# Optimization experiments

Measured on AMD Instinct MI355X. Metric: run time of the kernel, lower is better.

The kernel has to match this reference:

```python
import jax, jax.numpy as jnp
import numpy as np

B, L, D = 512, 128, 128  # batch, sequence_length (=k), embedding_dim==hidden_dim
C_CLIP = 10.0  # pointer logit clipping constant from Attention(C=10)


def _lstm_cell(x, h, c, w_ih, w_hh, b_ih, b_hh):
    # torch.nn.LSTMCell gate order: i, f, g, o
    gates = x @ w_ih.T + b_ih + h @ w_hh.T + b_hh
    i, f, g, o = jnp.split(gates, 4, axis=-1)
    c2 = jax.nn.sigmoid(f) * c + jax.nn.sigmoid(i) * jnp.tanh(g)
    h2 = jax.nn.sigmoid(o) * jnp.tanh(c2)
    return h2, c2


def setup_inputs() -> dict:
    key = jax.random.key(0)
    ks = jax.random.split(key, 16)
    s = 0.09  # ~1/sqrt(D) init scale
    return dict(
        decoder_input=jax.random.normal(ks[0], (B, D), jnp.float32),
        embedding_x=jax.random.normal(ks[1], (L, B, D), jnp.float32),
        h0=jax.random.normal(ks[2], (B, D), jnp.float32),
        c0=jax.random.normal(ks[3], (B, D), jnp.float32),
        encoder_output=jax.random.normal(ks[4], (L, B, D), jnp.float32),
        w_ih=jax.random.normal(ks[5], (4 * D, D), jnp.float32) * s,
        w_hh=jax.random.normal(ks[6], (4 * D, D), jnp.float32) * s,
        b_ih=jnp.zeros((4 * D,), jnp.float32),
        b_hh=jnp.zeros((4 * D,), jnp.float32),
        wq_p=jax.random.normal(ks[7], (D, D), jnp.float32) * s,
        bq_p=jnp.zeros((D,), jnp.float32),
        wr_p=jax.random.normal(ks[8], (D, D), jnp.float32) * s,
        br_p=jnp.zeros((D,), jnp.float32),
        v_p=jax.random.normal(ks[9], (D,), jnp.float32) * s,
        wq_g=jax.random.normal(ks[10], (D, D), jnp.float32) * s,
        bq_g=jnp.zeros((D,), jnp.float32),
        wr_g=jax.random.normal(ks[11], (D, D), jnp.float32) * s,
        br_g=jnp.zeros((D,), jnp.float32),
        v_g=jax.random.normal(ks[12], (D,), jnp.float32) * s,
    )


def _decode(decoder_input, embedding_x, h0, c0, encoder_output,
            w_ih, w_hh, b_ih, b_hh,
            wq_p, bq_p, wr_p, br_p, v_p,
            wq_g, bq_g, wr_g, br_g, v_g):
    enc = encoder_output.transpose(1, 0, 2)  # (B, L, D)
    emb = embedding_x.transpose(1, 0, 2)     # (B, L, D)
    # w_ref is a 1x1 Conv1d == per-position Linear; hoist out of the loop
    ref_p = enc @ wr_p.T + br_p              # (B, L, D) pointer refs
    ref_g = enc @ wr_g.T + br_g              # (B, L, D) glimpse refs
    barange = jnp.arange(B)

    mask0 = jnp.zeros((B, L), bool).at[:, :2].set(True)  # indices 0,1 pre-visited

    def step(carry, _):
        h, c, dec_in, mask, prev_idx, use_prev = carry
        h, c = _lstm_cell(dec_in, h, c, w_ih, w_hh, b_ih, b_hh)
        # mask_logit: only applied once prev_idx exists (i.e. after first step)
        mask_new = jnp.where(use_prev, mask.at[barange, prev_idx].set(True), mask)
        # glimpse attention (num_glimpse=1, no logit clipping)
        g = h
        u = jnp.einsum('d,bld->bl', v_g,
                       jnp.tanh(ref_g + (g @ wq_g.T + bq_g)[:, None, :]))
        u = jnp.where(use_prev & mask_new, -jnp.inf, u)
        p = jax.nn.softmax(u, axis=-1)
        g = jnp.einsum('bl,bld->bd', p, enc)  # glimpse readout uses raw encoder output
        # pointer attention (clipped logits)
        u = jnp.einsum('d,bld->bl', v_p,
                       jnp.tanh(ref_p + (g @ wq_p.T + bq_p)[:, None, :]))
        u = C_CLIP * jnp.tanh(u)
        u = jnp.where(use_prev & mask_new, -jnp.inf, u)
        probs = jax.nn.softmax(u, axis=-1)          # (B, L)
        idx = jnp.argmax(probs, axis=-1)            # greedy decode
        dec_in = emb[barange, idx]                  # (B, D)
        return (h, c, dec_in, mask_new, idx, jnp.array(True)), (probs, idx)

    init = (h0, c0, decoder_input, mask0,
            jnp.zeros((B,), jnp.int32), jnp.array(False))
    _, (probs_seq, idx_seq) = jax.lax.scan(step, init, None, length=L - 2)
    return probs_seq, idx_seq  # (L-2, B, L), (L-2, B)


def reference(decoder_input, embedding_x, h0, c0, encoder_output,
              w_ih, w_hh, b_ih, b_hh,
              wq_p, bq_p, wr_p, br_p, v_p,
              wq_g, bq_g, wr_g, br_g, v_g):
    return _decode(decoder_input, embedding_x, h0, c0, encoder_output,
                   w_ih, w_hh, b_ih, b_hh,
                   wq_p, bq_p, wr_p, br_p, v_p,
                   wq_g, bq_g, wr_g, br_g, v_g)
```

## Files before the change

### kernel.cpp

```cpp
#include <hip/hip_runtime.h>
#include <math.h>

namespace {

constexpr int kB = 512;
constexpr int kL = 128;
constexpr int kD = 128;
constexpr int kSteps = 126;

constexpr size_t OFF_WL   = 0;
constexpr size_t OFF_BIAS = 131072;
constexpr size_t OFF_WQLG = 131584;
constexpr size_t OFF_WQTP = 147968;
constexpr size_t OFF_WRTG = 164352;
constexpr size_t OFF_WRTP = 180736;
constexpr size_t OFF_WIHT = 197120;
constexpr size_t OFF_REFG = 262656;
constexpr size_t OFF_REFP = OFF_REFG + (size_t)kL * kB * kD;
constexpr size_t OFF_ENCQ = OFF_REFP + (size_t)kL * kB * kD;
constexpr size_t kTotalNoGx = OFF_ENCQ + (size_t)kL * kB * kD;
constexpr size_t OFF_GX   = kTotalNoGx;
constexpr size_t kTotalGx = OFF_GX + (size_t)129 * kB * 512;

constexpr size_t OUT_IDX_OFF = (size_t)kSteps * kB * kL;

constexpr int SM_REFP = 0;
constexpr int SM_H    = 16384;
constexpr int SM_C    = 16512;
constexpr int SM_G    = 16640;
constexpr int SM_RED  = 17152;
constexpr int SM_QG   = 17408;
constexpr int SM_U    = 17536;
constexpr int SM_PG   = 17664;
constexpr int SM_M    = 17792;
constexpr int SM_VG   = 17920;
constexpr int SM_VP   = 18048;
constexpr int SM_IDX  = 18176;
constexpr int SM_TOTAL= 18180;

__device__ __forceinline__ float tanh_fast(float x) {
  return 1.0f - __fdividef(2.0f, __expf(2.0f * x) + 1.0f);
}
__device__ __forceinline__ float sig_fast(float x) {
  return __fdividef(1.0f, 1.0f + __expf(-x));
}

#define KEEP4(v) asm volatile("" : "+v"(v.x), "+v"(v.y), "+v"(v.z), "+v"(v.w))

}

extern "C" __global__ void prep_weights(
    const float* __restrict__ w_ih, const float* __restrict__ w_hh,
    const float* __restrict__ b_ih, const float* __restrict__ b_hh,
    const float* __restrict__ wq_p, const float* __restrict__ wq_g,
    const float* __restrict__ wr_p, const float* __restrict__ wr_g,
    float* __restrict__ ws) {
  const int tid = blockIdx.x * blockDim.x + threadIdx.x;
  const int nth = gridDim.x * blockDim.x;
  for (int i = tid; i < 256 * 512; i += nth) {
    const int k = i >> 9, g = i & 511;
    ws[OFF_WL + i] = (k < 128) ? w_ih[g * 128 + k] : w_hh[g * 128 + (k - 128)];
  }
  for (int i = tid; i < 512; i += nth) ws[OFF_BIAS + i] = b_ih[i] + b_hh[i];
  for (int i = tid; i < 16384; i += nth) {
    const int e = i & 3, rest = i >> 2;
    const int kq = rest & 1, j = (rest >> 1) & 127, kk4 = rest >> 8;
    const int k = kq * 64 + kk4 * 4 + e;
    ws[OFF_WQLG + i] = wq_g[j * 128 + k];
  }
  for (int i = tid; i < 128 * 512; i += nth) {
    const int k = i >> 9, g = i & 511;
    ws[OFF_WIHT + i] = w_ih[g * 128 + k];
  }
  for (int i = tid; i < 128 * 128; i += nth) {
    const int k = i >> 7, j = i & 127;
    ws[OFF_WQTP + i] = wq_p[j * 128 + k];
    ws[OFF_WRTG + i] = wr_g[j * 128 + k];
    ws[OFF_WRTP + i] = wr_p[j * 128 + k];
  }
}

extern "C" __global__ __launch_bounds__(256) void prep_mm(
    const float* __restrict__ enc,
    const float* __restrict__ br_g, const float* __restrict__ br_p,
    const float* __restrict__ bq_p,
    float* __restrict__ ws) {
  extern __shared__ float lds[];
  float* wT = lds;
  float* sx = lds + 16384;
  const int t = threadIdx.x;
  const int table = blockIdx.y;
  const size_t wOff = (table == 0) ? OFF_WRTG : (table == 1) ? OFF_WRTP : OFF_WQTP;
  const size_t oOff = (table == 0) ? OFF_REFG : (table == 1) ? OFF_REFP : OFF_ENCQ;
  const float* bias = (table == 0) ? br_g : (table == 1) ? br_p : bq_p;
  for (int i = t; i < 16384; i += 256) wT[i] = ws[wOff + i];
  const size_t r0 = (size_t)blockIdx.x * 64;
  for (int i = t; i < 8192; i += 256) sx[i] = enc[r0 * 128 + i];
  __syncthreads();
  const int j0 = (t & 31) * 4, rg = t >> 5;
  float4 acc[8];
  const float4 b4 = *(const float4*)(bias + j0);
  #pragma unroll
  for (int r = 0; r < 8; ++r) acc[r] = b4;
  for (int k4 = 0; k4 < 32; ++k4) {
    const float4 w0 = *(const float4*)&wT[(k4 * 4 + 0) * 128 + j0];
    const float4 w1 = *(const float4*)&wT[(k4 * 4 + 1) * 128 + j0];
    const float4 w2 = *(const float4*)&wT[(k4 * 4 + 2) * 128 + j0];
    const float4 w3 = *(const float4*)&wT[(k4 * 4 + 3) * 128 + j0];
    #pragma unroll
    for (int r = 0; r < 8; ++r) {
      const float4 xv = *(const float4*)&sx[(rg * 8 + r) * 128 + k4 * 4];
      acc[r].x += xv.x * w0.x + xv.y * w1.x + xv.z * w2.x + xv.w * w3.x;
      acc[r].y += xv.x * w0.y + xv.y * w1.y + xv.z * w2.y + xv.w * w3.y;
      acc[r].z += xv.x * w0.z + xv.y * w1.z + xv.z * w2.z + xv.w * w3.z;
      acc[r].w += xv.x * w0.w + xv.y * w1.w + xv.z * w2.w + xv.w * w3.w;
    }
  }
  #pragma unroll
  for (int r = 0; r < 8; ++r) {
    *(float4*)&ws[oOff + (r0 + rg * 8 + r) * 128 + j0] = acc[r];
  }
}

extern "C" __global__ __launch_bounds__(256) void prep_gx(
    const float* __restrict__ emb, const float* __restrict__ dec0,
    float* __restrict__ ws) {
  extern __shared__ float lds[];
  float* wT = lds;
  float* sx = lds + 16384;
  const int t = threadIdx.x;
  const int g0 = blockIdx.y * 128;
  for (int i = t; i < 16384; i += 256) {
    wT[i] = ws[OFF_WIHT + (size_t)(i >> 7) * 512 + g0 + (i & 127)];
  }
  const size_t r0 = (size_t)blockIdx.x * 64;
  for (int i = t; i < 8192; i += 256) {
    const size_t rid = r0 + (i >> 7);
    const int c = i & 127;
    sx[i] = (rid < 65536) ? emb[rid * 128 + c] : dec0[(rid - 65536) * 128 + c];
  }
  __syncthreads();
  const int j0 = (t & 31) * 4, rg = t >> 5;
  float4 acc[8];
  const float4 b4 = *(const float4*)(ws + OFF_BIAS + g0 + j0);
  #pragma unroll
  for (int r = 0; r < 8; ++r) acc[r] = b4;
  for (int k4 = 0; k4 < 32; ++k4) {
    const float4 w0 = *(const float4*)&wT[(k4 * 4 + 0) * 128 + j0];
    const float4 w1 = *(const float4*)&wT[(k4 * 4 + 1) * 128 + j0];
    const float4 w2 = *(const float4*)&wT[(k4 * 4 + 2) * 128 + j0];
    const float4 w3 = *(const float4*)&wT[(k4 * 4 + 3) * 128 + j0];
    #pragma unroll
    for (int r = 0; r < 8; ++r) {
      const float4 xv = *(const float4*)&sx[(rg * 8 + r) * 128 + k4 * 4];
      acc[r].x += xv.x * w0.x + xv.y * w1.x + xv.z * w2.x + xv.w * w3.x;
      acc[r].y += xv.x * w0.y + xv.y * w1.y + xv.z * w2.y + xv.w * w3.y;
      acc[r].z += xv.x * w0.z + xv.y * w1.z + xv.z * w2.z + xv.w * w3.z;
      acc[r].w += xv.x * w0.w + xv.y * w1.w + xv.z * w2.w + xv.w * w3.w;
    }
  }
  #pragma unroll
  for (int r = 0; r < 8; ++r) {
    *(float4*)&ws[OFF_GX + (r0 + rg * 8 + r) * 512 + g0 + j0] = acc[r];
  }
}

template <bool GX>
__global__ __launch_bounds__(256, 2) void decode_main(
    const float* __restrict__ dec0, const float* __restrict__ emb,
    const float* __restrict__ h0,   const float* __restrict__ c0,
    const float* __restrict__ bq_g, const float* __restrict__ v_p,
    const float* __restrict__ v_g,
    const float* __restrict__ ws, float* __restrict__ out) {
  extern __shared__ float sm[];
  int* s_idx = (int*)(sm + SM_IDX);

  const int t = threadIdx.x;
  const int b = blockIdx.x;
  const int wv = t >> 6, lane = t & 63;
  const int sub = lane & 15, rr = lane >> 4;
  const int j2 = t >> 1, kq = t & 1;
  const int lh = t >> 7, dd = t & 127;

  #pragma unroll
  for (int it = 0; it < 8; ++it) {
    const int l = it * 16 + wv * 4 + rr;
    const float* src = ws + OFF_REFP + ((size_t)l * kB + b) * kD + sub * 8;
    *(float4*)&sm[SM_REFP + (it * 512 + t) * 4]       = *(const float4*)src;
    *(float4*)&sm[SM_REFP + (it * 512 + 256 + t) * 4] = *(const float4*)(src + 4);
  }
  if (t < 128) {
    sm[SM_H + t]  = h0[b * 128 + t];
    sm[SM_C + t]  = c0[b * 128 + t];
    sm[SM_M + t]  = (t < 2) ? 1.f : 0.f;
    sm[SM_VG + t] = v_g[t];
    sm[SM_VP + t] = v_p[t];
  }
  if (t == 0) *s_idx = 128;
  const float bqg = bq_g[j2];
  const float bias0 = ws[OFF_BIAS + 2 * t];
  const float bias1 = ws[OFF_BIAS + 2 * t + 1];
  __syncthreads();

  const float* WL  = ws + OFF_WL;
  const float* WHH = WL + 128 * 512;
  const float* WQG = ws + OFF_WQLG + 4 * t;
  const float* REFG = ws + OFF_REFG;
  const float* ENCQ = ws + OFF_ENCQ;
  const float* GXT  = ws + OFF_GX;

  const float* rgp0 = REFG + ((size_t)( 0 + wv * 4 + rr) * kB + b) * kD + sub * 8;
  const float* rgp1 = REFG + ((size_t)(16 + wv * 4 + rr) * kB + b) * kD + sub * 8;
  const float* rgp2 = REFG + ((size_t)(32 + wv * 4 + rr) * kB + b) * kD + sub * 8;
  const float* rgp3 = REFG + ((size_t)(48 + wv * 4 + rr) * kB + b) * kD + sub * 8;
  const float* rgp4 = REFG + ((size_t)(64 + wv * 4 + rr) * kB + b) * kD + sub * 8;
  const float* rgp5 = REFG + ((size_t)(80 + wv * 4 + rr) * kB + b) * kD + sub * 8;
  const float* rgp6 = REFG + ((size_t)(96 + wv * 4 + rr) * kB + b) * kD + sub * 8;
  const float* rgp7 = REFG + ((size_t)(112 + wv * 4 + rr) * kB + b) * kD + sub * 8;

  for (int step = 0; step < kSteps; ++step) {
    float4 ga0 = *(const float4*)rgp0, gb0 = *(const float4*)(rgp0 + 4);
    float4 ga1 = *(const float4*)rgp1, gb1 = *(const float4*)(rgp1 + 4);
    float4 ga2 = *(const float4*)rgp2, gb2 = *(const float4*)(rgp2 + 4);
    float4 ga3 = *(const float4*)rgp3, gb3 = *(const float4*)(rgp3 + 4);
    float4 ga4 = *(const float4*)rgp4, gb4 = *(const float4*)(rgp4 + 4);
    float4 ga5 = *(const float4*)rgp5, gb5 = *(const float4*)(rgp5 + 4);
    float4 ga6 = *(const float4*)rgp6, gb6 = *(const float4*)(rgp6 + 4);
    float4 ga7 = *(const float4*)rgp7, gb7 = *(const float4*)(rgp7 + 4);
    KEEP4(ga0); KEEP4(gb0); KEEP4(ga1); KEEP4(gb1);
    KEEP4(ga2); KEEP4(gb2); KEEP4(ga3); KEEP4(gb3);
    KEEP4(ga4); KEEP4(gb4); KEEP4(ga5); KEEP4(gb5);
    KEEP4(ga6); KEEP4(gb6); KEEP4(ga7); KEEP4(gb7);
    {
      float a0, a1;
      const int row = *s_idx;
      if constexpr (GX) {
        const float2 gx2 = *(const float2*)(GXT + ((size_t)row * kB + b) * 512 + 2 * t);
        a0 = gx2.x; a1 = gx2.y;
      } else {
        if (t < 128) {
          const float* xs = (row == 128) ? dec0 + (size_t)b * 128
                                         : emb + ((size_t)row * kB + b) * kD;
          sm[SM_RED + t] = xs[t];
        }
        __syncthreads();
        a0 = bias0; a1 = bias1;
        const float* wp = WL + 2 * t;
        #pragma unroll 8
        for (int k4 = 0; k4 < 32; ++k4) {
          const float4 x4 = *(const float4*)&sm[SM_RED + k4 * 4];
          const float2 w0 = *(const float2*)(wp + (size_t)(k4 * 4 + 0) * 512);
          const float2 w1 = *(const float2*)(wp + (size_t)(k4 * 4 + 1) * 512);
          const float2 w2 = *(const float2*)(wp + (size_t)(k4 * 4 + 2) * 512);
          const float2 w3 = *(const float2*)(wp + (size_t)(k4 * 4 + 3) * 512);
          a0 += x4.x * w0.x + x4.y * w1.x + x4.z * w2.x + x4.w * w3.x;
          a1 += x4.x * w0.y + x4.y * w1.y + x4.z * w2.y + x4.w * w3.y;
        }
      }
      const float* wp = WHH + 2 * t;
      #pragma unroll 8
      for (int k4 = 0; k4 < 32; ++k4) {
        const float4 h4 = *(const float4*)&sm[SM_H + k4 * 4];
        const float2 w0 = *(const float2*)(wp + (size_t)(k4 * 4 + 0) * 512);
        const float2 w1 = *(const float2*)(wp + (size_t)(k4 * 4 + 1) * 512);
        const float2 w2 = *(const float2*)(wp + (size_t)(k4 * 4 + 2) * 512);
        const float2 w3 = *(const float2*)(wp + (size_t)(k4 * 4 + 3) * 512);
        a0 += h4.x * w0.x + h4.y * w1.x + h4.z * w2.x + h4.w * w3.x;
        a1 += h4.x * w0.y + h4.y * w1.y + h4.z * w2.y + h4.w * w3.y;
      }
      *(float2*)&sm[SM_G + 2 * t] = make_float2(a0, a1);
    }
    __syncthreads();
    if (t < 128) {
      const float gi = sm[SM_G + t];
      const float gf = sm[SM_G + 128 + t];
      const float gg = sm[SM_G + 256 + t];
      const float go = sm[SM_G + 384 + t];
      const float cc = sig_fast(gf) * sm[SM_C + t] + sig_fast(gi) * tanh_fast(gg);
      sm[SM_C + t] = cc;
      sm[SM_H + t] = sig_fast(go) * tanh_fast(cc);
    } else if (t == 128 && step > 0) {
      sm[SM_M + *s_idx] = 1.f;
    }
    __syncthreads();
    {
      float acc = 0.f;
      #pragma unroll 4
      for (int kk4 = 0; kk4 < 16; ++kk4) {
        const float4 w  = *(const float4*)(WQG + (size_t)kk4 * 1024);
        const float4 h4 = *(const float4*)&sm[SM_H + kq * 64 + kk4 * 4];
        acc += h4.x * w.x + h4.y * w.y + h4.z * w.z + h4.w * w.w;
      }
      acc += __shfl_xor(acc, 1);
      if (!kq) sm[SM_QG + j2] = acc + bqg;
    }
    __syncthreads();
    {
      const float4 qa = *(const float4*)&sm[SM_QG + sub * 8];
      const float4 qb = *(const float4*)&sm[SM_QG + sub * 8 + 4];
      const float4 va = *(const float4*)&sm[SM_VG + sub * 8];
      const float4 vb = *(const float4*)&sm[SM_VG + sub * 8 + 4];
      #define P4_ROW(IT, RA, RB)                                            \
      {                                                                     \
        const int l = IT * 16 + wv * 4 + rr;                                \
        float s;                                                            \
        s  = va.x * tanh_fast(RA.x + qa.x);                                 \
        s += va.y * tanh_fast(RA.y + qa.y);                                 \
        s += va.z * tanh_fast(RA.z + qa.z);                                 \
        s += va.w * tanh_fast(RA.w + qa.w);                                 \
        s += vb.x * tanh_fast(RB.x + qb.x);                                 \
        s += vb.y * tanh_fast(RB.y + qb.y);                                 \
        s += vb.z * tanh_fast(RB.z + qb.z);                                 \
        s += vb.w * tanh_fast(RB.w + qb.w);                                 \
        s += __shfl_xor(s, 1); s += __shfl_xor(s, 2);                       \
        s += __shfl_xor(s, 4); s += __shfl_xor(s, 8);                       \
        if (sub == 0) {                                                     \
          if (step > 0 && sm[SM_M + l] != 0.f) s = -INFINITY;               \
          sm[SM_U + l] = s;                                                 \
        }                                                                   \
      }
      P4_ROW(0, ga0, gb0) P4_ROW(1, ga1, gb1)
      P4_ROW(2, ga2, gb2) P4_ROW(3, ga3, gb3)
      P4_ROW(4, ga4, gb4) P4_ROW(5, ga5, gb5)
      P4_ROW(6, ga6, gb6) P4_ROW(7, ga7, gb7)
      #undef P4_ROW
    }
    __syncthreads();
    if (t < 64) {
      const float v0 = sm[SM_U + t], v1 = sm[SM_U + 64 + t];
      float m = fmaxf(v0, v1);
      #pragma unroll
      for (int off = 1; off < 64; off <<= 1) m = fmaxf(m, __shfl_xor(m, off, 64));
      const float e0 = __expf(v0 - m), e1 = __expf(v1 - m);
      float ssum = e0 + e1;
      #pragma unroll
      for (int off = 1; off < 64; off <<= 1) ssum += __shfl_xor(ssum, off, 64);
      const float inv = __fdividef(1.0f, ssum);
      sm[SM_PG + t]      = e0 * inv;
      sm[SM_PG + 64 + t] = e1 * inv;
    }
    __syncthreads();
    {
      float acc = 0.f;
      #pragma unroll 8
      for (int ll = 0; ll < 64; ++ll) {
        const int l = lh * 64 + ll;
        acc += sm[SM_PG + l] * ENCQ[((size_t)l * kB + b) * kD + dd];
      }
      sm[SM_RED + t] = acc;
    }
    __syncthreads();
    {
      const float4 r0a = *(const float4*)&sm[SM_RED + sub * 8];
      const float4 r0b = *(const float4*)&sm[SM_RED + sub * 8 + 4];
      const float4 r1a = *(const float4*)&sm[SM_RED + 128 + sub * 8];
      const float4 r1b = *(const float4*)&sm[SM_RED + 128 + sub * 8 + 4];
      const float4 qa = make_float4(r0a.x + r1a.x, r0a.y + r1a.y,
                                    r0a.z + r1a.z, r0a.w + r1a.w);
      const float4 qb = make_float4(r0b.x + r1b.x, r0b.y + r1b.y,
                                    r0b.z + r1b.z, r0b.w + r1b.w);
      const float4 va = *(const float4*)&sm[SM_VP + sub * 8];
      const float4 vb = *(const float4*)&sm[SM_VP + sub * 8 + 4];
      #pragma unroll
      for (int it = 0; it < 8; ++it) {
        const int l = it * 16 + wv * 4 + rr;
        const float4 ra = *(const float4*)&sm[SM_REFP + (it * 512 + t) * 4];
        const float4 rb = *(const float4*)&sm[SM_REFP + (it * 512 + 256 + t) * 4];
        float s;
        s  = va.x * tanh_fast(ra.x + qa.x);
        s += va.y * tanh_fast(ra.y + qa.y);
        s += va.z * tanh_fast(ra.z + qa.z);
        s += va.w * tanh_fast(ra.w + qa.w);
        s += vb.x * tanh_fast(rb.x + qb.x);
        s += vb.y * tanh_fast(rb.y + qb.y);
        s += vb.z * tanh_fast(rb.z + qb.z);
        s += vb.w * tanh_fast(rb.w + qb.w);
        s += __shfl_xor(s, 1); s += __shfl_xor(s, 2);
        s += __shfl_xor(s, 4); s += __shfl_xor(s, 8);
        if (sub == 0) {
          float uu = 10.f * tanh_fast(s);
          if (step > 0 && sm[SM_M + l] != 0.f) uu = -INFINITY;
          sm[SM_U + l] = uu;
        }
      }
    }
    __syncthreads();
    if (t < 64) {
      const float v0 = sm[SM_U + t], v1 = sm[SM_U + 64 + t];
      float m = fmaxf(v0, v1);
      #pragma unroll
      for (int off = 1; off < 64; off <<= 1) m = fmaxf(m, __shfl_xor(m, off, 64));
      const float e0 = __expf(v0 - m), e1 = __expf(v1 - m);
      float ssum = e0 + e1;
      #pragma unroll
      for (int off = 1; off < 64; off <<= 1) ssum += __shfl_xor(ssum, off, 64);
      const float inv = __fdividef(1.0f, ssum);
      float* orow = out + ((size_t)step * kB + b) * kL;
      orow[t]      = e0 * inv;
      orow[64 + t] = e1 * inv;
      float av; int ai;
      if (v0 >= v1) { av = v0; ai = t; } else { av = v1; ai = t + 64; }
      #pragma unroll
      for (int off = 1; off < 64; off <<= 1) {
        const float ov = __shfl_xor(av, off, 64);
        const int   oi = __shfl_xor(ai, off, 64);
        if (ov > av || (ov == av && oi < ai)) { av = ov; ai = oi; }
      }
      if (t == 0) {
        *s_idx = ai;
        out[OUT_IDX_OFF + (size_t)step * kB + b] = (float)ai;
      }
    }
    __syncthreads();
  }
}

extern "C" void kernel_launch(void* const* d_in, const int* in_sizes, int n_in,
                              void* d_out, int out_size, void* d_ws, size_t ws_size,
                              hipStream_t stream) {
  (void)in_sizes; (void)n_in; (void)out_size;
  const float* dec0 = (const float*)d_in[0];
  const float* emb  = (const float*)d_in[1];
  const float* h0   = (const float*)d_in[2];
  const float* c0   = (const float*)d_in[3];
  const float* enc  = (const float*)d_in[4];
  const float* w_ih = (const float*)d_in[5];
  const float* w_hh = (const float*)d_in[6];
  const float* b_ih = (const float*)d_in[7];
  const float* b_hh = (const float*)d_in[8];
  const float* wq_p = (const float*)d_in[9];
  const float* bq_p = (const float*)d_in[10];
  const float* wr_p = (const float*)d_in[11];
  const float* br_p = (const float*)d_in[12];
  const float* v_p  = (const float*)d_in[13];
  const float* wq_g = (const float*)d_in[14];
  const float* bq_g = (const float*)d_in[15];
  const float* wr_g = (const float*)d_in[16];
  const float* br_g = (const float*)d_in[17];
  const float* v_g  = (const float*)d_in[18];
  float* ws  = (float*)d_ws;
  float* out = (float*)d_out;

  const bool gx_ok = ws_size >= kTotalGx * 4;

  prep_weights<<<dim3(64), dim3(256), 0, stream>>>(
      w_ih, w_hh, b_ih, b_hh, wq_p, wq_g, wr_p, wr_g, ws);
  prep_mm<<<dim3(1024, 3), dim3(256), 24576 * 4, stream>>>(
      enc, br_g, br_p, bq_p, ws);
  if (gx_ok) {
    prep_gx<<<dim3(1032, 4), dim3(256), 24576 * 4, stream>>>(emb, dec0, ws);
    decode_main<true><<<dim3(512), dim3(256), SM_TOTAL * 4, stream>>>(
        dec0, emb, h0, c0, bq_g, v_p, v_g, ws, out);
  } else {
    decode_main<false><<<dim3(512), dim3(256), SM_TOTAL * 4, stream>>>(
        dec0, emb, h0, c0, bq_g, v_p, v_g, ws, out);
  }
}
```

Baseline: 3.695 ms.

## Fold tanh scaling into weights and prefetch encoder rows into registers

Rewrites the tanh-based attention scores as sum(v) - 2*sum(v/(exp2(k*x)+1)). The 2*log2(e) factor is pre-multiplied into the glimpse and pointer projections and their biases, so each element needs only a raw v_exp_f32 and v_rcp_f32 with no division or extra multiply. Separately, the 64 encoder values used by the glimpse-weighted sum are loaded into registers at the start of each step, so their latency overlaps the LSTM and glimpse computations instead of stalling the reduction loop. The trade-off is heavy register pressure from the 64-element array, which may lower occupancy, plus slightly different rounding from the raw hardware transcendentals.

```diff
diff --git a/kernel.cpp b/kernel.cpp
--- a/kernel.cpp
+++ b/kernel.cpp
@@ -7,6 +7,7 @@
 constexpr int kL = 128;
 constexpr int kD = 128;
 constexpr int kSteps = 126;
+constexpr float kK = 2.8853900817779268f;
 
 constexpr size_t OFF_WL   = 0;
 constexpr size_t OFF_BIAS = 131072;
@@ -44,8 +45,15 @@
 __device__ __forceinline__ float sig_fast(float x) {
   return __fdividef(1.0f, 1.0f + __expf(-x));
 }
+__device__ __forceinline__ float exp2_raw(float x) {
+  float r; asm("v_exp_f32 %0, %1" : "=v"(r) : "v"(x)); return r;
+}
+__device__ __forceinline__ float rcp_raw(float x) {
+  float r; asm("v_rcp_f32 %0, %1" : "=v"(r) : "v"(x)); return r;
+}
 
 #define KEEP4(v) asm volatile("" : "+v"(v.x), "+v"(v.y), "+v"(v.z), "+v"(v.w))
+#define KEEP1(v) asm volatile("" : "+v"(v))
 
 }
 
@@ -66,7 +74,7 @@
     const int e = i & 3, rest = i >> 2;
     const int kq = rest & 1, j = (rest >> 1) & 127, kk4 = rest >> 8;
     const int k = kq * 64 + kk4 * 4 + e;
-    ws[OFF_WQLG + i] = wq_g[j * 128 + k];
+    ws[OFF_WQLG + i] = kK * wq_g[j * 128 + k];
   }
   for (int i = tid; i < 128 * 512; i += nth) {
     const int k = i >> 9, g = i & 511;
@@ -118,6 +126,7 @@
   }
   #pragma unroll
   for (int r = 0; r < 8; ++r) {
+    acc[r].x *= kK; acc[r].y *= kK; acc[r].z *= kK; acc[r].w *= kK;
     *(float4*)&ws[oOff + (r0 + rg * 8 + r) * 128 + j0] = acc[r];
   }
 }
@@ -193,14 +202,24 @@
     sm[SM_H + t]  = h0[b * 128 + t];
     sm[SM_C + t]  = c0[b * 128 + t];
     sm[SM_M + t]  = (t < 2) ? 1.f : 0.f;
-    sm[SM_VG + t] = v_g[t];
-    sm[SM_VP + t] = v_p[t];
+    sm[SM_VG + t] = 2.0f * v_g[t];
+    sm[SM_VP + t] = 2.0f * v_p[t];
   }
   if (t == 0) *s_idx = 128;
-  const float bqg = bq_g[j2];
+  const float bqg = kK * bq_g[j2];
   const float bias0 = ws[OFF_BIAS + 2 * t];
   const float bias1 = ws[OFF_BIAS + 2 * t + 1];
   __syncthreads();
+
+  float vgsum = 0.f, vpsum = 0.f;
+  #pragma unroll 8
+  for (int i = 0; i < 128; i += 4) {
+    const float4 a = *(const float4*)&sm[SM_VG + i];
+    const float4 p = *(const float4*)&sm[SM_VP + i];
+    vgsum += a.x + a.y + a.z + a.w;
+    vpsum += p.x + p.y + p.z + p.w;
+  }
+  vgsum *= 0.5f; vpsum *= 0.5f;
 
   const float* WL  = ws + OFF_WL;
   const float* WHH = WL + 128 * 512;
@@ -217,6 +236,7 @@
   const float* rgp5 = REFG + ((size_t)(80 + wv * 4 + rr) * kB + b) * kD + sub * 8;
   const float* rgp6 = REFG + ((size_t)(96 + wv * 4 + rr) * kB + b) * kD + sub * 8;
   const float* rgp7 = REFG + ((size_t)(112 + wv * 4 + rr) * kB + b) * kD + sub * 8;
+  const float* eqp  = ENCQ + (size_t)lh * 64 * kB * kD + (size_t)b * kD + dd;
 
   for (int step = 0; step < kSteps; ++step) {
     float4 ga0 = *(const float4*)rgp0, gb0 = *(const float4*)(rgp0 + 4);
@@ -227,10 +247,17 @@
     float4 ga5 = *(const float4*)rgp5, gb5 = *(const float4*)(rgp5 + 4);
     float4 ga6 = *(const float4*)rgp6, gb6 = *(const float4*)(rgp6 + 4);
     float4 ga7 = *(const float4*)rgp7, gb7 = *(const float4*)(rgp7 + 4);
+    float eqv[64];
+    #pragma unroll
+    for (int ll = 0; ll < 64; ++ll) {
+      eqv[ll] = eqp[(size_t)ll * kB * kD];
+    }
     KEEP4(ga0); KEEP4(gb0); KEEP4(ga1); KEEP4(gb1);
     KEEP4(ga2); KEEP4(gb2); KEEP4(ga3); KEEP4(gb3);
     KEEP4(ga4); KEEP4(gb4); KEEP4(ga5); KEEP4(gb5);
     KEEP4(ga6); KEEP4(gb6); KEEP4(ga7); KEEP4(gb7);
+    #pragma unroll
+    for (int ll = 0; ll < 64; ++ll) KEEP1(eqv[ll]);
     {
       float a0, a1;
       const int row = *s_idx;
@@ -303,20 +330,21 @@
       #define P4_ROW(IT, RA, RB)                                            \
       {                                                                     \
         const int l = IT * 16 + wv * 4 + rr;                                \
-        float s;                                                            \
-        s  = va.x * tanh_fast(RA.x + qa.x);                                 \
-        s += va.y * tanh_fast(RA.y + qa.y);                                 \
-        s += va.z * tanh_fast(RA.z + qa.z);                                 \
-        s += va.w * tanh_fast(RA.w + qa.w);                                 \
-        s += vb.x * tanh_fast(RB.x + qb.x);                                 \
-        s += vb.y * tanh_fast(RB.y + qb.y);                                 \
-        s += vb.z * tanh_fast(RB.z + qb.z);                                 \
-        s += vb.w * tanh_fast(RB.w + qb.w);                                 \
-        s += __shfl_xor(s, 1); s += __shfl_xor(s, 2);                       \
-        s += __shfl_xor(s, 4); s += __shfl_xor(s, 8);                       \
+        float s2;                                                           \
+        s2  = va.x * rcp_raw(exp2_raw(RA.x + qa.x) + 1.0f);                 \
+        s2 += va.y * rcp_raw(exp2_raw(RA.y + qa.y) + 1.0f);                 \
+        s2 += va.z * rcp_raw(exp2_raw(RA.z + qa.z) + 1.0f);                 \
+        s2 += va.w * rcp_raw(exp2_raw(RA.w + qa.w) + 1.0f);                 \
+        s2 += vb.x * rcp_raw(exp2_raw(RB.x + qb.x) + 1.0f);                 \
+        s2 += vb.y * rcp_raw(exp2_raw(RB.y + qb.y) + 1.0f);                 \
+        s2 += vb.z * rcp_raw(exp2_raw(RB.z + qb.z) + 1.0f);                 \
+        s2 += vb.w * rcp_raw(exp2_raw(RB.w + qb.w) + 1.0f);                 \
+        s2 += __shfl_xor(s2, 1); s2 += __shfl_xor(s2, 2);                   \
+        s2 += __shfl_xor(s2, 4); s2 += __shfl_xor(s2, 8);                   \
         if (sub == 0) {                                                     \
-          if (step > 0 && sm[SM_M + l] != 0.f) s = -INFINITY;               \
-          sm[SM_U + l] = s;                                                 \
+          float u = vgsum - s2;                                             \
+          if (step > 0 && sm[SM_M + l] != 0.f) u = -INFINITY;               \
+          sm[SM_U + l] = u;                                                 \
         }                                                                   \
       }
       P4_ROW(0, ga0, gb0) P4_ROW(1, ga1, gb1)
@@ -342,10 +370,9 @@
     __syncthreads();
     {
       float acc = 0.f;
-      #pragma unroll 8
+      #pragma unroll
       for (int ll = 0; ll < 64; ++ll) {
-        const int l = lh * 64 + ll;
-        acc += sm[SM_PG + l] * ENCQ[((size_t)l * kB + b) * kD + dd];
+        acc += sm[SM_PG + lh * 64 + ll] * eqv[ll];
       }
       sm[SM_RED + t] = acc;
     }
@@ -366,19 +393,19 @@
         const int l = it * 16 + wv * 4 + rr;
         const float4 ra = *(const float4*)&sm[SM_REFP + (it * 512 + t) * 4];
         const float4 rb = *(const float4*)&sm[SM_REFP + (it * 512 + 256 + t) * 4];
-        float s;
-        s  = va.x * tanh_fast(ra.x + qa.x);
-        s += va.y * tanh_fast(ra.y + qa.y);
-        s += va.z * tanh_fast(ra.z + qa.z);
-        s += va.w * tanh_fast(ra.w + qa.w);
-        s += vb.x * tanh_fast(rb.x + qb.x);
-        s += vb.y * tanh_fast(rb.y + qb.y);
-        s += vb.z * tanh_fast(rb.z + qb.z);
-        s += vb.w * tanh_fast(rb.w + qb.w);
-        s += __shfl_xor(s, 1); s += __shfl_xor(s, 2);
-        s += __shfl_xor(s, 4); s += __shfl_xor(s, 8);
+        float s2;
+        s2  = va.x * rcp_raw(exp2_raw(ra.x + qa.x) + 1.0f);
+        s2 += va.y * rcp_raw(exp2_raw(ra.y + qa.y) + 1.0f);
+        s2 += va.z * rcp_raw(exp2_raw(ra.z + qa.z) + 1.0f);
+        s2 += va.w * rcp_raw(exp2_raw(ra.w + qa.w) + 1.0f);
+        s2 += vb.x * rcp_raw(exp2_raw(rb.x + qb.x) + 1.0f);
+        s2 += vb.y * rcp_raw(exp2_raw(rb.y + qb.y) + 1.0f);
+        s2 += vb.z * rcp_raw(exp2_raw(rb.z + qb.z) + 1.0f);
+        s2 += vb.w * rcp_raw(exp2_raw(rb.w + qb.w) + 1.0f);
+        s2 += __shfl_xor(s2, 1); s2 += __shfl_xor(s2, 2);
+        s2 += __shfl_xor(s2, 4); s2 += __shfl_xor(s2, 8);
         if (sub == 0) {
-          float uu = 10.f * tanh_fast(s);
+          float uu = 10.f * tanh_fast(vpsum - s2);
           if (step > 0 && sm[SM_M + l] != 0.f) uu = -INFINITY;
           sm[SM_U + l] = uu;
         }
```

Result: slower. 6.978 ms (+88.9%).
